# Optimization experiments

Hardware: AMD Instinct MI355X
Metric: run time of the kernel (lower is better)

## Reference

```python
import jax, jax.numpy as jnp
import numpy as np
from jax import lax

NB, HH, WW, C = 8, 64, 64, 192
G, K, DW_K, PA_K = 12, 3, 5, 3
GC, P = C // G, K * K
PAD, STRIDE, DIL = 1, 1, 1
OFFSET_SCALE = 1.0
LN_EPS = 1e-5


def _grid_sample(img, grid):
    # img: (B,Cc,H,W); grid: (B,L,P,2) xy in [-1,1]; bilinear, zeros padding, align_corners=False
    B, Cc, H, W = img.shape
    gx = (grid[..., 0] + 1.0) * (W * 0.5) - 0.5
    gy = (grid[..., 1] + 1.0) * (H * 0.5) - 0.5
    x0, y0 = jnp.floor(gx), jnp.floor(gy)

    def gather(xi, yi):
        valid = (xi >= 0) & (xi <= W - 1) & (yi >= 0) & (yi <= H - 1)
        xc = jnp.clip(xi, 0, W - 1).astype(jnp.int32)
        yc = jnp.clip(yi, 0, H - 1).astype(jnp.int32)
        v = jax.vmap(lambda im, y, x: im[:, y, x])(img, yc, xc)  # (B,Cc,L,P)
        return v * valid[:, None].astype(img.dtype)

    wx1, wy1 = gx - x0, gy - y0
    wx0, wy0 = 1.0 - wx1, 1.0 - wy1
    return (gather(x0, y0) * (wx0 * wy0)[:, None]
            + gather(x0 + 1.0, y0) * (wx1 * wy0)[:, None]
            + gather(x0, y0 + 1.0) * (wx0 * wy1)[:, None]
            + gather(x0 + 1.0, y0 + 1.0) * (wx1 * wy1)[:, None])


def _dcnv3_core(x, offset, mask):
    # x: (N,H,W,C) projected input; offset: (N,H,W,G*P*2); mask: (N,H,W,G*P)
    N, H, W, _ = x.shape
    xp = jnp.pad(x, ((0, 0), (PAD, PAD), (PAD, PAD), (0, 0)))
    Hp, Wp = H + 2 * PAD, W + 2 * PAD
    Ho, Wo = offset.shape[1], offset.shape[2]
    base = (DIL * (K - 1)) // 2 + 0.5
    ref_y = (base + jnp.arange(Ho) * STRIDE) / Hp
    ref_x = (base + jnp.arange(Wo) * STRIDE) / Wp
    ref = jnp.stack(jnp.broadcast_arrays(ref_x[None, :], ref_y[:, None]), -1)  # (Ho,Wo,2) xy
    start = -((DIL * (K - 1)) // 2)
    pts = (start + jnp.arange(K) * DIL).astype(x.dtype)
    gxg = jnp.broadcast_to((pts / Wp)[:, None], (K, K))  # w offset varies along dim0 (torch order)
    gyg = jnp.broadcast_to((pts / Hp)[None, :], (K, K))
    grid = jnp.tile(jnp.stack([gxg, gyg], -1).reshape(P, 2), (G, 1))  # (G*P,2)
    loc = ref[None, :, :, None, :] + grid * OFFSET_SCALE  # (1,Ho,Wo,G*P,2)
    norm = jnp.array([Wp, Hp], dtype=x.dtype)
    loc = loc + offset.reshape(N, Ho, Wo, G * P, 2) * OFFSET_SCALE / norm
    sg = 2.0 * loc - 1.0  # (N,Ho,Wo,G*P,2)
    img = xp.reshape(N, Hp * Wp, G, GC).transpose(0, 2, 3, 1).reshape(N * G, GC, Hp, Wp)
    grd = sg.reshape(N, Ho * Wo, G, P, 2).transpose(0, 2, 1, 3, 4).reshape(N * G, Ho * Wo, P, 2)
    samp = _grid_sample(img, grd)  # (N*G, GC, L, P)
    m = mask.reshape(N, Ho * Wo, G, P).transpose(0, 2, 1, 3).reshape(N * G, 1, Ho * Wo, P)
    out = (samp * m).sum(-1)  # (N*G, GC, L)
    return out.reshape(N, G, GC, Ho * Wo).transpose(0, 3, 1, 2).reshape(N, Ho, Wo, C)


def _dcnv3(x, dw_w, dw_b, ln_g, ln_b, off_w, off_b, msk_w, msk_b, in_w, in_b, out_w, out_b, cfs_w, cfs_b):
    N, H, W, _ = x.shape
    x_proj = x @ in_w + in_b
    # depthwise conv (5x5) -> LayerNorm (channels_last) -> GELU(exact)
    u = lax.conv_general_dilated(x, dw_w, (1, 1), 'SAME',
                                 dimension_numbers=('NHWC', 'HWIO', 'NHWC'),
                                 feature_group_count=C) + dw_b
    mu = u.mean(-1, keepdims=True)
    var = ((u - mu) ** 2).mean(-1, keepdims=True)
    u = (u - mu) * lax.rsqrt(var + LN_EPS) * ln_g + ln_b
    u = jax.nn.gelu(u, approximate=False)
    offset = u @ off_w + off_b  # (N,H,W,G*P*2)
    m = jax.nn.softmax((u @ msk_w + msk_b).reshape(N, H, W, G, P), axis=-1).reshape(N, H, W, G * P)
    y = _dcnv3_core(x_proj, offset, m)
    cfs = jax.nn.sigmoid(u @ cfs_w + cfs_b)  # (N,H,W,G)
    cfs = jnp.repeat(cfs, GC, axis=-1)       # (N,H,W,C), group-blockwise
    y = y * (1.0 - cfs) + x_proj * cfs
    return y @ out_w + out_b


def _patch_attention(x):
    # x: (N,H,W,C) -> std over softmax'd 3x3 neighbor scores: (N,H,W)
    N, H, W, _ = x.shape
    pad = (PA_K - 1) // 2
    xp = jnp.pad(x, ((0, 0), (pad, pad), (pad, pad), (0, 0)))
    neigh = jnp.stack([xp[:, i:i + H, j:j + W, :] for i in range(PA_K) for j in range(PA_K)],
                      axis=-1)  # (N,H,W,C,K1*K2), torch unfold ordering
    scores = jnp.einsum('nhwc,nhwck->nhwk', x, neigh)
    sm = jax.nn.softmax(scores, axis=-1)
    return jnp.std(sm, axis=-1, ddof=1)  # torch.std is unbiased


def setup_inputs() -> dict:
    key = jax.random.key(0)
    ks = jax.random.split(key, 8)
    s = 0.02
    return {
        'x': jax.random.normal(ks[0], (NB, HH, WW, C), jnp.float32),
        'dw_w': jax.random.normal(ks[1], (DW_K, DW_K, 1, C), jnp.float32) * s,
        'dw_b': jnp.zeros((C,), jnp.float32),
        'ln_g': jnp.ones((C,), jnp.float32),
        'ln_b': jnp.zeros((C,), jnp.float32),
        'off_w': jax.random.normal(ks[2], (C, G * P * 2), jnp.float32) * s,
        'off_b': jnp.zeros((G * P * 2,), jnp.float32),
        'msk_w': jax.random.normal(ks[3], (C, G * P), jnp.float32) * s,
        'msk_b': jnp.zeros((G * P,), jnp.float32),
        'in_w': jax.random.normal(ks[4], (C, C), jnp.float32) * s,
        'in_b': jnp.zeros((C,), jnp.float32),
        'out_w': jax.random.normal(ks[5], (C, C), jnp.float32) * s,
        'out_b': jnp.zeros((C,), jnp.float32),
        'cfs_w': jax.random.normal(ks[6], (C, G), jnp.float32) * s,
        'cfs_b': jnp.zeros((G,), jnp.float32),
    }


def reference(x, dw_w, dw_b, ln_g, ln_b, off_w, off_b, msk_w, msk_b, in_w, in_b, out_w, out_b, cfs_w, cfs_b):
    x1 = _dcnv3(x, dw_w, dw_b, ln_g, ln_b, off_w, off_b, msk_w, msk_b, in_w, in_b, out_w, out_b, cfs_w, cfs_b)
    mask = _patch_attention(x1)           # (N,H,W)
    return x + x1 * mask[..., None]
```

## Files before the change

kernel.cpp:

```cpp
#include <hip/hip_runtime.h>
#include <hip/hip_bf16.h>
#include <math.h>

#define NB 8
#define HH 64
#define WW 64
#define C 192
#define G 12
#define GC 16
#define P 9
#define NPIX (NB*HH*WW)

typedef __attribute__((ext_vector_type(8))) short short8;
typedef __attribute__((ext_vector_type(4))) float f32x4;
typedef unsigned short ushort;

__device__ __forceinline__ ushort to_bf16(float f) {
  __hip_bfloat16 b = __float2bfloat16(f);
  return *(ushort*)&b;
}
__device__ __forceinline__ float bf2f(ushort u) {
  union { unsigned u; float f; } cv; cv.u = ((unsigned)u) << 16; return cv.f;
}
__device__ __forceinline__ float bflo(unsigned u) {
  union { unsigned v; float f; } c; c.v = u << 16; return c.f;
}
__device__ __forceinline__ float bfhi(unsigned u) {
  union { unsigned v; float f; } c; c.v = u & 0xffff0000u; return c.f;
}

__global__ void prep_w_kernel(const float* __restrict__ in_w, const float* __restrict__ out_w,
    const float* __restrict__ off_w, const float* __restrict__ msk_w, const float* __restrict__ cfs_w,
    const float* __restrict__ off_b, const float* __restrict__ msk_b, const float* __restrict__ cfs_b,
    ushort* __restrict__ in_wt, ushort* __restrict__ out_wt, ushort* __restrict__ wf_t,
    float* __restrict__ bf_bias) {
  int idx = blockIdx.x*256 + threadIdx.x;
  if (idx < 36864) {
    int n = idx/192, k = idx%192;
    in_wt[idx] = to_bf16(in_w[k*192 + n]);
  } else if (idx < 73728) {
    int j = idx - 36864; int n = j/192, k = j%192;
    out_wt[j] = to_bf16(out_w[k*192 + n]);
  } else if (idx < 147456) {
    int j = idx - 73728; int n = j/192, k = j%192;
    float v = 0.f;
    if (n < 216)      v = off_w[k*216 + n];
    else if (n < 324) v = msk_w[k*108 + (n-216)];
    else if (n < 336) v = cfs_w[k*12  + (n-324)];
    wf_t[j] = to_bf16(v);
  }
  if (idx < 384) {
    float b = 0.f;
    if (idx < 216)      b = off_b[idx];
    else if (idx < 324) b = msk_b[idx-216];
    else if (idx < 336) b = cfs_b[idx-324];
    bf_bias[idx] = b;
  }
}

template<int NW, int NSTORE, bool BF16OUT, bool AF32>
__global__ __launch_bounds__(256) void mfma_gemm(const void* __restrict__ A_,
    const ushort* __restrict__ Wt, const float* __restrict__ bias,
    void* __restrict__ Cout_) {
  __shared__ ushort As[4*64*8];
  __shared__ ushort Bs[4*64*8];
  int pix0 = blockIdx.x * 64, n0 = blockIdx.y * 64;
  int tid = threadIdx.x;
  int wid = tid >> 6, lane = tid & 63;
  int wr = wid >> 1, wc = wid & 1;
  int lr = lane >> 4, lc = lane & 15;

  f32x4 acc[2][2];
  #pragma unroll
  for (int m=0;m<2;m++)
    #pragma unroll
    for (int j=0;j<2;j++) acc[m][j] = (f32x4){0.f,0.f,0.f,0.f};

  int s_kb = tid >> 6, s_row = tid & 63;

  short8 pa, pb;
  auto load_tile = [&](int k0) {
    if (AF32) {
      const float* Af = (const float*)A_;
      float4 u0 = *(const float4*)&Af[(size_t)(pix0 + s_row)*192 + k0 + s_kb*8];
      float4 u1 = *(const float4*)&Af[(size_t)(pix0 + s_row)*192 + k0 + s_kb*8 + 4];
      pa[0]=to_bf16(u0.x); pa[1]=to_bf16(u0.y); pa[2]=to_bf16(u0.z); pa[3]=to_bf16(u0.w);
      pa[4]=to_bf16(u1.x); pa[5]=to_bf16(u1.y); pa[6]=to_bf16(u1.z); pa[7]=to_bf16(u1.w);
    } else {
      const ushort* Ab = (const ushort*)A_;
      pa = *(const short8*)&Ab[(size_t)(pix0 + s_row)*192 + k0 + s_kb*8];
    }
    pb = *(const short8*)&Wt[(size_t)(n0 + s_row)*192 + k0 + s_kb*8];
  };
  load_tile(0);

  for (int t = 0; t < 6; t++) {
    __syncthreads();
    *(short8*)&As[(size_t)tid*8] = pa;
    *(short8*)&Bs[(size_t)tid*8] = pb;
    __syncthreads();
    if (t < 5) load_tile((t+1)*32);
    short8 a0 = *(const short8*)&As[(size_t)(lr*64 + wr*32 + lc)*8];
    short8 a1 = *(const short8*)&As[(size_t)(lr*64 + wr*32 + 16 + lc)*8];
    short8 b0 = *(const short8*)&Bs[(size_t)(lr*64 + wc*32 + lc)*8];
    short8 b1 = *(const short8*)&Bs[(size_t)(lr*64 + wc*32 + 16 + lc)*8];
    acc[0][0] = __builtin_amdgcn_mfma_f32_16x16x32_bf16(a0, b0, acc[0][0], 0,0,0);
    acc[0][1] = __builtin_amdgcn_mfma_f32_16x16x32_bf16(a0, b1, acc[0][1], 0,0,0);
    acc[1][0] = __builtin_amdgcn_mfma_f32_16x16x32_bf16(a1, b0, acc[1][0], 0,0,0);
    acc[1][1] = __builtin_amdgcn_mfma_f32_16x16x32_bf16(a1, b1, acc[1][1], 0,0,0);
  }
  #pragma unroll
  for (int j=0;j<2;j++) {
    int col = n0 + wc*32 + j*16 + lc;
    if (NW != NSTORE && col >= NSTORE) continue;
    float bb = bias[col];
    #pragma unroll
    for (int m=0;m<2;m++) {
      size_t rbase = pix0 + wr*32 + m*16 + lr*4;
      #pragma unroll
      for (int r=0;r<4;r++) {
        float v = acc[m][j][r] + bb;
        if (BF16OUT) ((ushort*)Cout_)[(rbase + r)*NSTORE + col] = to_bf16(v);
        else         ((float*) Cout_)[(rbase + r)*NSTORE + col] = v;
      }
    }
  }
}

#define SEG 16
__global__ __launch_bounds__(192) void dw_ln_gelu_kernel(const float* __restrict__ x,
    const float* __restrict__ dw_w, const float* __restrict__ dw_b,
    const float* __restrict__ ln_g, const float* __restrict__ ln_b,
    ushort* __restrict__ u_out) {
  int bid = blockIdx.x;
  int blk = (bid & 7) * 256 + (bid >> 3);
  int qw = blk & 3; int nh = blk >> 2;
  int h = nh & 63, n = nh >> 6;
  int c = threadIdx.x;
  int w0 = qw * SEG;

  float kw[25];
  #pragma unroll
  for (int t=0;t<25;t++) kw[t] = dw_w[t*C + c];

  float acc[SEG];
  float bb = dw_b[c];
  #pragma unroll
  for (int i=0;i<SEG;i++) acc[i] = bb;

  #pragma unroll
  for (int i=0;i<5;i++) {
    int hy = h + i - 2;
    if (hy < 0 || hy >= HH) continue;
    const float* rowp = &x[(((size_t)n*HH + hy)*WW)*C + c];
    #pragma unroll
    for (int wi=0; wi<SEG+4; wi++) {
      int w_in = w0 - 2 + wi;
      if (w_in < 0 || w_in >= WW) continue;
      float v = rowp[(size_t)w_in*C];
      #pragma unroll
      for (int j=0;j<5;j++) {
        int a = wi - j;
        if (a >= 0 && a < SEG) acc[a] += v * kw[i*5+j];
      }
    }
  }

  __shared__ float lds_acc[SEG][C+1];
  __shared__ float part1[SEG][12], part2[SEG][12];
  __shared__ float mu_s[SEG], rs_s[SEG];
  #pragma unroll
  for (int i=0;i<SEG;i++) lds_acc[i][c] = acc[i];
  __syncthreads();
  {
    int p = threadIdx.x & 15, chunk = threadIdx.x >> 4;
    float s1 = 0.f, s2 = 0.f;
    #pragma unroll
    for (int k=0;k<16;k++) {
      float v = lds_acc[p][chunk*16 + k];
      s1 += v; s2 += v*v;
    }
    part1[p][chunk] = s1; part2[p][chunk] = s2;
  }
  __syncthreads();
  if (threadIdx.x < SEG) {
    int p = threadIdx.x;
    float t1 = 0.f, t2 = 0.f;
    #pragma unroll
    for (int k=0;k<12;k++){ t1 += part1[p][k]; t2 += part2[p][k]; }
    float mu = t1 * (1.0f/C);
    float var = t2 * (1.0f/C) - mu*mu;
    mu_s[p] = mu; rs_s[p] = rsqrtf(var + 1e-5f);
  }
  __syncthreads();
  float gg = ln_g[c], lb = ln_b[c];
  size_t obase = ((size_t)nh*WW + w0)*C + c;
  #pragma unroll
  for (int i=0;i<SEG;i++) {
    float uv = (acc[i] - mu_s[i])*rs_s[i]*gg + lb;
    uv = 0.5f*uv*(1.0f + erff(uv*0.70710678118654752f));
    u_out[obase + (size_t)i*C] = to_bf16(uv);
  }
}

#define SPX 8
__device__ __forceinline__ void fma8(float* acc, float w, uint4 q) {
  acc[0] += w*bflo(q.x); acc[1] += w*bfhi(q.x);
  acc[2] += w*bflo(q.y); acc[3] += w*bfhi(q.y);
  acc[4] += w*bflo(q.z); acc[5] += w*bfhi(q.z);
  acc[6] += w*bflo(q.w); acc[7] += w*bfhi(q.w);
}
__global__ __launch_bounds__(192) void sample_kernel(const ushort* __restrict__ omc,
    const ushort* __restrict__ x_proj, ushort* __restrict__ y_out) {
  int bid = blockIdx.x;
  int swz = (bid & 7) * 512 + (bid >> 3);
  int pix0 = swz * SPX;
  int n = pix0 >> 12;
  int hw = pix0 & 4095; int h = hw >> 6; int w0 = hw & 63;
  int tid = threadIdx.x;
  __shared__ int    addrs[SPX*108*4];
  __shared__ ushort wts16[SPX*108*4];
  __shared__ float  cfss[SPX][12];

  for (int i = tid; i < SPX*108; i += 192) {
    int px = i / 108, gp = i % 108;
    int p = gp % 9;
    const float pts[3] = {-1.f, 0.f, 1.f};
    unsigned off2 = ((const unsigned*)omc)[(size_t)(pix0+px)*168 + gp];
    float ox = bflo(off2), oy = bfhi(off2);
    float gx = 1.0f + (float)(w0+px) + pts[p/3] + ox;
    float gy = 1.0f + (float)h + pts[p%3] + oy;
    float x0f = floorf(gx), y0f = floorf(gy);
    float wx1 = gx - x0f, wy1 = gy - y0f;
    float wx0 = 1.f-wx1, wy0 = 1.f-wy1;
    int x0 = (int)x0f, y0 = (int)y0f;
    bool xv0 = (x0   >= 1) && (x0   <= 64);
    bool xv1 = (x0+1 >= 1) && (x0+1 <= 64);
    bool yv0 = (y0   >= 1) && (y0   <= 64);
    bool yv1 = (y0+1 >= 1) && (y0+1 <= 64);
    int base = n*HH*WW*C;
    int4 a4;
    a4.x = (yv0&&xv0) ? (base + ((y0-1)*WW + (x0-1))*C)*2 : 0;
    a4.y = (yv0&&xv1) ? (base + ((y0-1)*WW + (x0  ))*C)*2 : 0;
    a4.z = (yv1&&xv0) ? (base + ((y0  )*WW + (x0-1))*C)*2 : 0;
    a4.w = (yv1&&xv1) ? (base + ((y0  )*WW + (x0  ))*C)*2 : 0;
    ((int4*)addrs)[i] = a4;
    ushort4 w4;
    w4.x = to_bf16((yv0&&xv0) ? wx0*wy0 : 0.f);
    w4.y = to_bf16((yv0&&xv1) ? wx1*wy0 : 0.f);
    w4.z = to_bf16((yv1&&xv0) ? wx0*wy1 : 0.f);
    w4.w = to_bf16((yv1&&xv1) ? wx1*wy1 : 0.f);
    ((ushort4*)wts16)[i] = w4;
  }
  __syncthreads();
  if (tid < SPX*12) {
    int px = tid / 12, gg = tid % 12;
    const ushort* mrow = &omc[(size_t)(pix0+px)*336 + 216 + gg*9];
    float lv[P];
    #pragma unroll
    for (int p=0;p<P;p++) lv[p] = bf2f(mrow[p]);
    float m = -1e30f;
    #pragma unroll
    for (int p=0;p<P;p++) m = fmaxf(m, lv[p]);
    float s = 0.f;
    #pragma unroll
    for (int p=0;p<P;p++){ lv[p] = expf(lv[p]-m); s += lv[p]; }
    float cf = 1.0f/(1.0f+expf(-bf2f(omc[(size_t)(pix0+px)*336 + 324 + gg])));
    cfss[px][gg] = cf;
    float onem = (1.0f - cf) / s;
    #pragma unroll
    for (int p=0;p<P;p++) {
      int i = px*108 + gg*9 + p;
      float mp = lv[p]*onem;
      ushort4 w4 = ((const ushort4*)wts16)[i];
      w4.x = to_bf16(bf2f(w4.x)*mp);
      w4.y = to_bf16(bf2f(w4.y)*mp);
      w4.z = to_bf16(bf2f(w4.z)*mp);
      w4.w = to_bf16(bf2f(w4.w)*mp);
      ((ushort4*)wts16)[i] = w4;
    }
  }
  __syncthreads();
  int px = tid / 24, s = tid - (tid/24)*24;
  int g = s >> 1;
  int cb = s * 16;
  const char* xb = (const char*)x_proj;
  float acc[8] = {0.f,0.f,0.f,0.f,0.f,0.f,0.f,0.f};
  #pragma unroll
  for (int pb = 0; pb < 3; pb++) {
    int gp = g*9 + pb*3;
    int4 a0 = ((const int4*)addrs)[px*108+gp];
    int4 a1 = ((const int4*)addrs)[px*108+gp+1];
    int4 a2 = ((const int4*)addrs)[px*108+gp+2];
    ushort4 u0 = ((const ushort4*)wts16)[px*108+gp];
    ushort4 u1 = ((const ushort4*)wts16)[px*108+gp+1];
    ushort4 u2 = ((const ushort4*)wts16)[px*108+gp+2];
    uint4 t00 = *(const uint4*)(xb + (unsigned)(a0.x + cb));
    uint4 t01 = *(const uint4*)(xb + (unsigned)(a0.y + cb));
    uint4 t02 = *(const uint4*)(xb + (unsigned)(a0.z + cb));
    uint4 t03 = *(const uint4*)(xb + (unsigned)(a0.w + cb));
    uint4 t10 = *(const uint4*)(xb + (unsigned)(a1.x + cb));
    uint4 t11 = *(const uint4*)(xb + (unsigned)(a1.y + cb));
    uint4 t12 = *(const uint4*)(xb + (unsigned)(a1.z + cb));
    uint4 t13 = *(const uint4*)(xb + (unsigned)(a1.w + cb));
    uint4 t20 = *(const uint4*)(xb + (unsigned)(a2.x + cb));
    uint4 t21 = *(const uint4*)(xb + (unsigned)(a2.y + cb));
    uint4 t22 = *(const uint4*)(xb + (unsigned)(a2.z + cb));
    uint4 t23 = *(const uint4*)(xb + (unsigned)(a2.w + cb));
    fma8(acc, bf2f(u0.x), t00); fma8(acc, bf2f(u0.y), t01);
    fma8(acc, bf2f(u0.z), t02); fma8(acc, bf2f(u0.w), t03);
    fma8(acc, bf2f(u1.x), t10); fma8(acc, bf2f(u1.y), t11);
    fma8(acc, bf2f(u1.z), t12); fma8(acc, bf2f(u1.w), t13);
    fma8(acc, bf2f(u2.x), t20); fma8(acc, bf2f(u2.y), t21);
    fma8(acc, bf2f(u2.z), t22); fma8(acc, bf2f(u2.w), t23);
  }
  float cf = cfss[px][g];
  uint4 qx = *(const uint4*)(xb + ((size_t)(pix0+px)*C)*2 + cb);
  fma8(acc, cf, qx);
  short8 r;
  #pragma unroll
  for (int k=0;k<8;k++) r[k] = to_bf16(acc[k]);
  *(short8*)&y_out[(size_t)(pix0+px)*C + s*8] = r;
}

__global__ __launch_bounds__(256) void pattn_kernel(const float* __restrict__ x,
    const ushort* __restrict__ x1, float* __restrict__ out) {
  __shared__ unsigned xs[100*97];
  __shared__ float psc[64][36];
  __shared__ float sd_s[64];
  int blk = blockIdx.x;
  int n = blk >> 6;
  int ty = (blk >> 3) & 7, tx = blk & 7;
  int th0 = ty*8, tw0 = tx*8;
  int tid = threadIdx.x;
  const unsigned* x1u = (const unsigned*)x1;
  for (int i = tid; i < 100*96; i += 256) {
    int cell = i / 96, wd = i - cell*96;
    int gy = th0 - 1 + cell/10, gx = tw0 - 1 + cell%10;
    unsigned v = 0;
    if (gy>=0 && gy<HH && gx>=0 && gx<WW)
      v = x1u[(((size_t)n*HH+gy)*WW+gx)*96 + wd];
    xs[cell*97 + wd] = v;
  }
  __syncthreads();
  {
    int px = tid >> 2, qq = tid & 3;
    int py = px >> 3, pxx = px & 7;
    int cell = (py+1)*10 + (pxx+1);
    float cen[48];
    #pragma unroll
    for (int k=0;k<24;k++) {
      unsigned w = xs[cell*97 + qq*24 + k];
      cen[2*k] = bflo(w); cen[2*k+1] = bfhi(w);
    }
    #pragma unroll
    for (int ni=0;ni<9;ni++) {
      int nc = cell + (ni/3-1)*10 + (ni%3-1);
      float a = 0.f;
      #pragma unroll
      for (int k=0;k<24;k++) {
        unsigned w = xs[nc*97 + qq*24 + k];
        a += cen[2*k]*bflo(w) + cen[2*k+1]*bfhi(w);
      }
      psc[px][qq*9+ni] = a;
    }
  }
  __syncthreads();
  if (tid < 64) {
    float sc[9];
    #pragma unroll
    for (int k=0;k<9;k++)
      sc[k] = psc[tid][k] + psc[tid][9+k] + psc[tid][18+k] + psc[tid][27+k];
    float m = sc[0];
    #pragma unroll
    for (int k=1;k<9;k++) m = fmaxf(m, sc[k]);
    float pr[9]; float s = 0.f;
    #pragma unroll
    for (int k=0;k<9;k++){ pr[k] = expf(sc[k]-m); s += pr[k]; }
    float inv = 1.0f/s;
    float mean = 0.f;
    #pragma unroll
    for (int k=0;k<9;k++){ pr[k] *= inv; mean += pr[k]; }
    mean *= (1.0f/9.0f);
    float var = 0.f;
    #pragma unroll
    for (int k=0;k<9;k++){ float d = pr[k]-mean; var += d*d; }
    sd_s[tid] = sqrtf(var*(1.0f/8.0f));
  }
  __syncthreads();
  for (int i = tid; i < 64*96; i += 256) {
    int p2 = i / 96, wd = i - p2*96;
    int py2 = p2 >> 3, px2 = p2 & 7;
    unsigned v = xs[((py2+1)*10 + (px2+1))*97 + wd];
    size_t pix = ((size_t)n*HH + th0+py2)*WW + tw0+px2;
    float2 xv = ((const float2*)x)[pix*96 + wd];
    float sd = sd_s[p2];
    float2 o; o.x = xv.x + bflo(v)*sd; o.y = xv.y + bfhi(v)*sd;
    ((float2*)out)[pix*96 + wd] = o;
  }
}

extern "C" void kernel_launch(void* const* d_in, const int* in_sizes, int n_in,
                              void* d_out, int out_size, void* d_ws, size_t ws_size,
                              hipStream_t stream) {
  const float* x     = (const float*)d_in[0];
  const float* dw_w  = (const float*)d_in[1];
  const float* dw_b  = (const float*)d_in[2];
  const float* ln_g  = (const float*)d_in[3];
  const float* ln_b  = (const float*)d_in[4];
  const float* off_w = (const float*)d_in[5];
  const float* off_b = (const float*)d_in[6];
  const float* msk_w = (const float*)d_in[7];
  const float* msk_b = (const float*)d_in[8];
  const float* in_w  = (const float*)d_in[9];
  const float* in_b  = (const float*)d_in[10];
  const float* out_w = (const float*)d_in[11];
  const float* out_b = (const float*)d_in[12];
  const float* cfs_w = (const float*)d_in[13];
  const float* cfs_b = (const float*)d_in[14];
  float* outp = (float*)d_out;

  ushort* omc    = (ushort*)d_ws;
  ushort* xproj  = omc + (size_t)NPIX*336;
  ushort* x1_bf  = xproj + (size_t)NPIX*192;
  ushort* u_bf   = x1_bf + (size_t)NPIX*192;
  ushort* in_wt  = u_bf + (size_t)NPIX*192;
  ushort* out_wt = in_wt + 192*192;
  ushort* wf_t   = out_wt + 192*192;
  float*  bfb    = (float*)(wf_t + 384*192);

  prep_w_kernel<<<(147456+255)/256, 256, 0, stream>>>(in_w, out_w, off_w, msk_w, cfs_w,
                                                       off_b, msk_b, cfs_b,
                                                       in_wt, out_wt, wf_t, bfb);
  mfma_gemm<192,192,true,true><<<dim3(NPIX/64, 3), 256, 0, stream>>>(x, in_wt, in_b, xproj);
  dw_ln_gelu_kernel<<<NB*HH*4, 192, 0, stream>>>(x, dw_w, dw_b, ln_g, ln_b, u_bf);
  mfma_gemm<384,336,true,false><<<dim3(NPIX/64, 6), 256, 0, stream>>>(u_bf, wf_t, bfb, omc);
  sample_kernel<<<NPIX/SPX, 192, 0, stream>>>(omc, xproj, u_bf);
  mfma_gemm<192,192,true,false><<<dim3(NPIX/64, 3), 256, 0, stream>>>(u_bf, out_wt, out_b, x1_bf);
  pattn_kernel<<<NB*64, 256, 0, stream>>>(x, x1_bf, outp);
}
```

Measured before the change: 149.9 us.

## Split deformable sampling into softmax prep kernel and smem-free gather kernel

Moves the mask softmax and sigmoid gating into a separate kernel that writes the combined modulation weights and gate values to workspace. The bilinear sampling kernel then drops its shared-memory staging and two block barriers, and each thread computes its own offsets, corner addresses and weights in registers. This cuts shared-memory traffic and synchronisation and may raise occupancy. In exchange it adds an extra launch, global round trips for the prep outputs, and redundant coordinate math since the two threads in each group repeat the same work. The per-pixel block swizzle is also removed.

Result: slower. 158.1 us (+5.5%).

```diff
diff --git a/kernel.cpp b/kernel.cpp
--- a/kernel.cpp
+++ b/kernel.cpp
@@ -203,124 +203,84 @@
   }
 }
 
-#define SPX 8
+__global__ __launch_bounds__(256) void smprep_kernel(const ushort* __restrict__ omc,
+    ushort* __restrict__ msm_pre, float* __restrict__ cfss) {
+  int idx = blockIdx.x*256 + threadIdx.x;
+  int px = idx / 12, g = idx % 12;
+  const ushort* mrow = &omc[(size_t)px*336 + 216 + g*9];
+  float lv[P];
+  #pragma unroll
+  for (int p=0;p<P;p++) lv[p] = bf2f(mrow[p]);
+  float m = lv[0];
+  #pragma unroll
+  for (int p=1;p<P;p++) m = fmaxf(m, lv[p]);
+  float s = 0.f;
+  #pragma unroll
+  for (int p=0;p<P;p++){ lv[p] = expf(lv[p]-m); s += lv[p]; }
+  float cf = 1.0f/(1.0f+expf(-bf2f(omc[(size_t)px*336 + 324 + g])));
+  cfss[idx] = cf;
+  float onem = (1.0f - cf) / s;
+  #pragma unroll
+  for (int p=0;p<P;p++)
+    msm_pre[(size_t)px*108 + g*9 + p] = to_bf16(lv[p]*onem);
+}
+
 __device__ __forceinline__ void fma8(float* acc, float w, uint4 q) {
   acc[0] += w*bflo(q.x); acc[1] += w*bfhi(q.x);
   acc[2] += w*bflo(q.y); acc[3] += w*bfhi(q.y);
   acc[4] += w*bflo(q.z); acc[5] += w*bfhi(q.z);
   acc[6] += w*bflo(q.w); acc[7] += w*bfhi(q.w);
 }
-__global__ __launch_bounds__(192) void sample_kernel(const ushort* __restrict__ omc,
+__global__ __launch_bounds__(256) void gather_kernel(const ushort* __restrict__ omc,
+    const ushort* __restrict__ msm_pre, const float* __restrict__ cfss,
     const ushort* __restrict__ x_proj, ushort* __restrict__ y_out) {
-  int bid = blockIdx.x;
-  int swz = (bid & 7) * 512 + (bid >> 3);
-  int pix0 = swz * SPX;
-  int n = pix0 >> 12;
-  int hw = pix0 & 4095; int h = hw >> 6; int w0 = hw & 63;
-  int tid = threadIdx.x;
-  __shared__ int    addrs[SPX*108*4];
-  __shared__ ushort wts16[SPX*108*4];
-  __shared__ float  cfss[SPX][12];
-
-  for (int i = tid; i < SPX*108; i += 192) {
-    int px = i / 108, gp = i % 108;
-    int p = gp % 9;
-    const float pts[3] = {-1.f, 0.f, 1.f};
-    unsigned off2 = ((const unsigned*)omc)[(size_t)(pix0+px)*168 + gp];
+  int idx = blockIdx.x*256 + threadIdx.x;
+  int px = idx / 24, s = idx - (idx/24)*24;
+  int g = s >> 1;
+  int n = px >> 12; int hw = px & 4095; int h = hw >> 6; int w = hw & 63;
+  int cb = s * 16;
+  const char* xb = (const char*)x_proj;
+  const unsigned* omc32 = (const unsigned*)omc;
+  int base = n*HH*WW*C;
+  const float pts[3] = {-1.f, 0.f, 1.f};
+  float acc[8] = {0.f,0.f,0.f,0.f,0.f,0.f,0.f,0.f};
+  #pragma unroll
+  for (int p=0;p<P;p++){
+    unsigned off2 = omc32[(size_t)px*168 + g*9 + p];
     float ox = bflo(off2), oy = bfhi(off2);
-    float gx = 1.0f + (float)(w0+px) + pts[p/3] + ox;
+    float gx = 1.0f + (float)w + pts[p/3] + ox;
     float gy = 1.0f + (float)h + pts[p%3] + oy;
     float x0f = floorf(gx), y0f = floorf(gy);
     float wx1 = gx - x0f, wy1 = gy - y0f;
     float wx0 = 1.f-wx1, wy0 = 1.f-wy1;
     int x0 = (int)x0f, y0 = (int)y0f;
-    bool xv0 = (x0   >= 1) && (x0   <= 64);
-    bool xv1 = (x0+1 >= 1) && (x0+1 <= 64);
-    bool yv0 = (y0   >= 1) && (y0   <= 64);
-    bool yv1 = (y0+1 >= 1) && (y0+1 <= 64);
-    int base = n*HH*WW*C;
-    int4 a4;
-    a4.x = (yv0&&xv0) ? (base + ((y0-1)*WW + (x0-1))*C)*2 : 0;
-    a4.y = (yv0&&xv1) ? (base + ((y0-1)*WW + (x0  ))*C)*2 : 0;
-    a4.z = (yv1&&xv0) ? (base + ((y0  )*WW + (x0-1))*C)*2 : 0;
-    a4.w = (yv1&&xv1) ? (base + ((y0  )*WW + (x0  ))*C)*2 : 0;
-    ((int4*)addrs)[i] = a4;
-    ushort4 w4;
-    w4.x = to_bf16((yv0&&xv0) ? wx0*wy0 : 0.f);
-    w4.y = to_bf16((yv0&&xv1) ? wx1*wy0 : 0.f);
-    w4.z = to_bf16((yv1&&xv0) ? wx0*wy1 : 0.f);
-    w4.w = to_bf16((yv1&&xv1) ? wx1*wy1 : 0.f);
-    ((ushort4*)wts16)[i] = w4;
-  }
-  __syncthreads();
-  if (tid < SPX*12) {
-    int px = tid / 12, gg = tid % 12;
-    const ushort* mrow = &omc[(size_t)(pix0+px)*336 + 216 + gg*9];
-    float lv[P];
-    #pragma unroll
-    for (int p=0;p<P;p++) lv[p] = bf2f(mrow[p]);
-    float m = -1e30f;
-    #pragma unroll
-    for (int p=0;p<P;p++) m = fmaxf(m, lv[p]);
-    float s = 0.f;
-    #pragma unroll
-    for (int p=0;p<P;p++){ lv[p] = expf(lv[p]-m); s += lv[p]; }
-    float cf = 1.0f/(1.0f+expf(-bf2f(omc[(size_t)(pix0+px)*336 + 324 + gg])));
-    cfss[px][gg] = cf;
-    float onem = (1.0f - cf) / s;
-    #pragma unroll
-    for (int p=0;p<P;p++) {
-      int i = px*108 + gg*9 + p;
-      float mp = lv[p]*onem;
-      ushort4 w4 = ((const ushort4*)wts16)[i];
-      w4.x = to_bf16(bf2f(w4.x)*mp);
-      w4.y = to_bf16(bf2f(w4.y)*mp);
-      w4.z = to_bf16(bf2f(w4.z)*mp);
-      w4.w = to_bf16(bf2f(w4.w)*mp);
-      ((ushort4*)wts16)[i] = w4;
-    }
-  }
-  __syncthreads();
-  int px = tid / 24, s = tid - (tid/24)*24;
-  int g = s >> 1;
-  int cb = s * 16;
-  const char* xb = (const char*)x_proj;
-  float acc[8] = {0.f,0.f,0.f,0.f,0.f,0.f,0.f,0.f};
-  #pragma unroll
-  for (int pb = 0; pb < 3; pb++) {
-    int gp = g*9 + pb*3;
-    int4 a0 = ((const int4*)addrs)[px*108+gp];
-    int4 a1 = ((const int4*)addrs)[px*108+gp+1];
-    int4 a2 = ((const int4*)addrs)[px*108+gp+2];
-    ushort4 u0 = ((const ushort4*)wts16)[px*108+gp];
-    ushort4 u1 = ((const ushort4*)wts16)[px*108+gp+1];
-    ushort4 u2 = ((const ushort4*)wts16)[px*108+gp+2];
-    uint4 t00 = *(const uint4*)(xb + (unsigned)(a0.x + cb));
-    uint4 t01 = *(const uint4*)(xb + (unsigned)(a0.y + cb));
-    uint4 t02 = *(const uint4*)(xb + (unsigned)(a0.z + cb));
-    uint4 t03 = *(const uint4*)(xb + (unsigned)(a0.w + cb));
-    uint4 t10 = *(const uint4*)(xb + (unsigned)(a1.x + cb));
-    uint4 t11 = *(const uint4*)(xb + (unsigned)(a1.y + cb));
-    uint4 t12 = *(const uint4*)(xb + (unsigned)(a1.z + cb));
-    uint4 t13 = *(const uint4*)(xb + (unsigned)(a1.w + cb));
-    uint4 t20 = *(const uint4*)(xb + (unsigned)(a2.x + cb));
-    uint4 t21 = *(const uint4*)(xb + (unsigned)(a2.y + cb));
-    uint4 t22 = *(const uint4*)(xb + (unsigned)(a2.z + cb));
-    uint4 t23 = *(const uint4*)(xb + (unsigned)(a2.w + cb));
-    fma8(acc, bf2f(u0.x), t00); fma8(acc, bf2f(u0.y), t01);
-    fma8(acc, bf2f(u0.z), t02); fma8(acc, bf2f(u0.w), t03);
-    fma8(acc, bf2f(u1.x), t10); fma8(acc, bf2f(u1.y), t11);
-    fma8(acc, bf2f(u1.z), t12); fma8(acc, bf2f(u1.w), t13);
-    fma8(acc, bf2f(u2.x), t20); fma8(acc, bf2f(u2.y), t21);
-    fma8(acc, bf2f(u2.z), t22); fma8(acc, bf2f(u2.w), t23);
-  }
-  float cf = cfss[px][g];
-  uint4 qx = *(const uint4*)(xb + ((size_t)(pix0+px)*C)*2 + cb);
+    bool xv0 = (x0 >= 1) && (x0 <= 64);
+    bool xv1 = (x0 >= 0) && (x0 <= 63);
+    bool yv0 = (y0 >= 1) && (y0 <= 64);
+    bool yv1 = (y0 >= 0) && (y0 <= 63);
+    float m = bf2f(msm_pre[(size_t)px*108 + g*9 + p]);
+    int a00 = (yv0&&xv0) ? (base + ((y0-1)*WW + (x0-1))*C)*2 : 0;
+    int a01 = (yv0&&xv1) ? (base + ((y0-1)*WW + (x0  ))*C)*2 : 0;
+    int a10 = (yv1&&xv0) ? (base + ((y0  )*WW + (x0-1))*C)*2 : 0;
+    int a11 = (yv1&&xv1) ? (base + ((y0  )*WW + (x0  ))*C)*2 : 0;
+    float w00 = (yv0&&xv0) ? wx0*wy0*m : 0.f;
+    float w01 = (yv0&&xv1) ? wx1*wy0*m : 0.f;
+    float w10 = (yv1&&xv0) ? wx0*wy1*m : 0.f;
+    float w11 = (yv1&&xv1) ? wx1*wy1*m : 0.f;
+    uint4 t0 = *(const uint4*)(xb + (unsigned)(a00 + cb));
+    uint4 t1 = *(const uint4*)(xb + (unsigned)(a01 + cb));
+    uint4 t2 = *(const uint4*)(xb + (unsigned)(a10 + cb));
+    uint4 t3 = *(const uint4*)(xb + (unsigned)(a11 + cb));
+    fma8(acc, w00, t0); fma8(acc, w01, t1);
+    fma8(acc, w10, t2); fma8(acc, w11, t3);
+  }
+  float cf = cfss[px*12 + g];
+  uint4 qx = *(const uint4*)(xb + ((size_t)px*C)*2 + cb);
   fma8(acc, cf, qx);
   short8 r;
   #pragma unroll
   for (int k=0;k<8;k++) r[k] = to_bf16(acc[k]);
-  *(short8*)&y_out[(size_t)(pix0+px)*C + s*8] = r;
+  *(short8*)&y_out[(size_t)px*C + s*8] = r;
 }
 
 __global__ __launch_bounds__(256) void pattn_kernel(const float* __restrict__ x,
@@ -420,14 +380,16 @@
   const float* cfs_b = (const float*)d_in[14];
   float* outp = (float*)d_out;
 
-  ushort* omc    = (ushort*)d_ws;
-  ushort* xproj  = omc + (size_t)NPIX*336;
-  ushort* x1_bf  = xproj + (size_t)NPIX*192;
-  ushort* u_bf   = x1_bf + (size_t)NPIX*192;
-  ushort* in_wt  = u_bf + (size_t)NPIX*192;
-  ushort* out_wt = in_wt + 192*192;
-  ushort* wf_t   = out_wt + 192*192;
-  float*  bfb    = (float*)(wf_t + 384*192);
+  ushort* omc     = (ushort*)d_ws;
+  ushort* xproj   = omc + (size_t)NPIX*336;
+  ushort* x1_bf   = xproj + (size_t)NPIX*192;
+  ushort* u_bf    = x1_bf + (size_t)NPIX*192;
+  ushort* msm_pre = u_bf + (size_t)NPIX*192;
+  float*  cfss    = (float*)(msm_pre + (size_t)NPIX*108);
+  ushort* in_wt   = (ushort*)(cfss + (size_t)NPIX*12);
+  ushort* out_wt  = in_wt + 192*192;
+  ushort* wf_t    = out_wt + 192*192;
+  float*  bfb     = (float*)(wf_t + 384*192);
 
   prep_w_kernel<<<(147456+255)/256, 256, 0, stream>>>(in_w, out_w, off_w, msk_w, cfs_w,
                                                        off_b, msk_b, cfs_b,
@@ -435,7 +397,8 @@
   mfma_gemm<192,192,true,true><<<dim3(NPIX/64, 3), 256, 0, stream>>>(x, in_wt, in_b, xproj);
   dw_ln_gelu_kernel<<<NB*HH*4, 192, 0, stream>>>(x, dw_w, dw_b, ln_g, ln_b, u_bf);
   mfma_gemm<384,336,true,false><<<dim3(NPIX/64, 6), 256, 0, stream>>>(u_bf, wf_t, bfb, omc);
-  sample_kernel<<<NPIX/SPX, 192, 0, stream>>>(omc, xproj, u_bf);
+  smprep_kernel<<<NPIX*12/256, 256, 0, stream>>>(omc, msm_pre, cfss);
+  gather_kernel<<<NPIX*24/256, 256, 0, stream>>>(omc, msm_pre, cfss, xproj, u_bf);
   mfma_gemm<192,192,true,false><<<dim3(NPIX/64, 3), 256, 0, stream>>>(u_bf, out_wt, out_b, x1_bf);
   pattn_kernel<<<NB*64, 256, 0, stream>>>(x, x1_bf, outp);
 }
```
